# Kernel tuning notes

Hardware: AMD Instinct MI355X
Metric: run time of the kernel (lower is better)

Reference implementation:

```python
import jax, jax.numpy as jnp
import numpy as np

L, B, D = 512, 16, 256
H = 4            # MAX_DIFF == num_heads
MAX_BONDS = 6
MAX_DIFF = 4
PROB_SHIFT = 0.3


def _attn_weights(x, Wqk, Wq, bq, Wk, bk, mask):
    """Per-head softmax(QK^T/sqrt(hd)) with key padding mask.
    x: [b,l,d]; Wqk: [d,2d] (the inc/dec_qk pre-projection);
    Wq/Wk: [d,d] (MHA in_proj, stored x@W layout); mask: [b,l] bool (True=masked).
    Returns [b,h,l,l]. The V path / out_proj of the torch MHA are discarded
    by the original module, so they are omitted here.
    """
    b, l, d = x.shape
    hd = d // H
    q = x @ Wqk[:, :d]
    k = x @ Wqk[:, d:]
    Q = (q @ Wq + bq).reshape(b, l, H, hd)
    K = (k @ Wk + bk).reshape(b, l, H, hd)
    scores = jnp.einsum('blhd,bmhd->bhlm', Q, K) / np.sqrt(hd)
    scores = jnp.where(mask[:, None, None, :], -jnp.inf, scores)
    return jax.nn.softmax(scores, axis=-1)


def setup_inputs() -> dict:
    key = jax.random.key(0)
    ks = jax.random.split(key, 16)
    s = 0.05
    p = lambda k, shape: jax.random.normal(k, shape, jnp.float32) * s
    # key_padding_mask: last 64 positions padded (True == masked)
    src_mask = jnp.broadcast_to(jnp.arange(L)[None, :] >= (L - 64), (B, L))
    return {
        'molecule_embedding': jax.random.normal(ks[0], (L, B, D), jnp.float32),
        'src_bond': jax.random.randint(ks[1], (B, L, MAX_BONDS), 0, L, jnp.int32),
        'src_mask': src_mask,
        'W_inc_qk': p(ks[2], (D, 2 * D)),
        'Wq_inc': p(ks[3], (D, D)), 'bq_inc': p(ks[4], (D,)),
        'Wk_inc': p(ks[5], (D, D)), 'bk_inc': p(ks[6], (D,)),
        'W_dec_qk': p(ks[7], (D, 2 * D)),
        'Wq_dec': p(ks[8], (D, D)), 'bq_dec': p(ks[9], (D,)),
        'Wk_dec': p(ks[10], (D, D)), 'bk_dec': p(ks[11], (D,)),
        'Wc': p(ks[12], (MAX_DIFF, MAX_DIFF)), 'bc': p(ks[13], (MAX_DIFF,)),
    }


def reference(molecule_embedding, src_bond, src_mask,
              W_inc_qk, Wq_inc, bq_inc, Wk_inc, bk_inc,
              W_dec_qk, Wq_dec, bq_dec, Wk_dec, bk_dec,
              Wc, bc):
    x = jnp.transpose(molecule_embedding, (1, 0, 2))  # [b,l,d]
    b, l, _ = x.shape

    inc = _attn_weights(x, W_inc_qk, Wq_inc, bq_inc, Wk_inc, bk_inc, src_mask)
    dec = _attn_weights(x, W_dec_qk, Wq_dec, bq_dec, Wk_dec, bk_dec, src_mask)

    pad = (~src_mask).astype(jnp.float32)              # 1 - mask
    pm2 = pad[:, :, None] * pad[:, None, :]            # [b,l,l]

    # cls_layer((inc-dec).permute(0,2,3,1)) * (MAX_DIFF*pad_mask)[...,None]
    diff = (jnp.einsum('bhlm,hc->blmc', inc - dec, Wc) + bc)
    diff = diff * (MAX_DIFF * pm2)[..., None]          # [b,l,l,4]

    # src_bond has last dim == MAX_BONDS -> one-hot neighbor counts
    src_w = jax.nn.one_hot(src_bond, l, dtype=jnp.float32).sum(axis=2) * pm2  # [b,l,l]
    eye = jnp.eye(l, dtype=jnp.float32)
    src_w = src_w * (1.0 - eye)[None]                  # zero diagonal

    # _shift_probs(src_weight.long(), prob_shift, MAX_DIFF)
    oh = jax.nn.one_hot(src_w.astype(jnp.int32), MAX_DIFF, dtype=jnp.float32)
    probs = oh * (1.0 - PROB_SHIFT) + (1.0 - oh) * (PROB_SHIFT / (MAX_DIFF - 1))
    probs = probs / probs.sum(axis=-1, keepdims=True)

    return jnp.log(probs + 1e-6) + diff                # [b,l,l,4]
```

## Files before the change

### kernel.cpp

```cpp
#include <hip/hip_runtime.h>
#include <stdint.h>

typedef unsigned short u16t;
typedef short s8v __attribute__((ext_vector_type(8)));
typedef float f4v __attribute__((ext_vector_type(4)));

#define MFMA16 __builtin_amdgcn_mfma_f32_16x16x32_bf16
#define QKN (16*4*512*64)

__device__ __forceinline__ u16t f2bf(float f) {
  unsigned u = __builtin_bit_cast(unsigned, f);
  u += 0x7fffu + ((u >> 16) & 1u);
  return (u16t)(u >> 16);
}

__global__ __launch_bounds__(256) void prep_kernel(
    const float* __restrict__ Wiqk, const float* __restrict__ Wqi, const float* __restrict__ Wki,
    const float* __restrict__ Wdqk, const float* __restrict__ Wqd, const float* __restrict__ Wkd,
    u16t* __restrict__ weffT, const int* __restrict__ mraw, int* __restrict__ mdst) {
  __shared__ float At[16][65];
  __shared__ float Bt[16][65];
  __shared__ int mode;
  const int tid = threadIdx.x;

  if (blockIdx.z == 4) {
    if (tid == 0) mode = 0;
    __syncthreads();
    unsigned v0 = (unsigned)mraw[tid], v1 = (unsigned)mraw[tid + 256];
    if (v0 == 0x3F800000u || v1 == 0x3F800000u) mode = 2;
    __syncthreads();
    if (mode == 0 && (v0 > 1u || v1 > 1u)) mode = 1;
    __syncthreads();
    const int g = blockIdx.y * 4 + blockIdx.x;
#pragma unroll
    for (int i = 0; i < 2; ++i) {
      int idx = g * 512 + i * 256 + tid;
      int m;
      if (mode == 2)      m = (((const float*)mraw)[idx] != 0.0f) ? 1 : 0;
      else if (mode == 1) m = ((const unsigned char*)mraw)[idx];
      else                m = mraw[idx];
      mdst[idx] = m;
    }
    return;
  }

  const int n0 = blockIdx.x * 64;
  const int d0 = blockIdx.y * 64;
  const int p  = blockIdx.z;
  const float* A2  = (p == 0) ? Wqi : (p == 1) ? Wki : (p == 2) ? Wqd : Wkd;
  const float* Wqk = (p < 2) ? Wiqk : Wdqk;
  const int aoff = (p & 1) * 256;
  const int tx = tid & 15, ty = tid >> 4;

  float acc[4][4];
#pragma unroll
  for (int i = 0; i < 4; ++i)
#pragma unroll
    for (int j = 0; j < 4; ++j) acc[i][j] = 0.f;

  for (int k0 = 0; k0 < 256; k0 += 16) {
    __syncthreads();
    {
      int nn = tid & 63, kr = tid >> 6;
#pragma unroll
      for (int pass = 0; pass < 4; ++pass) {
        int kk = kr + pass * 4;
        At[kk][nn] = A2[(size_t)(k0 + kk) * 256 + n0 + nn];
      }
      int kk = tid & 15, dr = tid >> 4;
#pragma unroll
      for (int pass = 0; pass < 4; ++pass) {
        int dd = dr + pass * 16;
        Bt[kk][dd] = Wqk[(size_t)(d0 + dd) * 512 + aoff + k0 + kk];
      }
    }
    __syncthreads();
#pragma unroll
    for (int kk = 0; kk < 16; ++kk) {
      float a[4], b[4];
#pragma unroll
      for (int i = 0; i < 4; ++i) a[i] = At[kk][ty * 4 + i];
#pragma unroll
      for (int j = 0; j < 4; ++j) b[j] = Bt[kk][tx * 4 + j];
#pragma unroll
      for (int i = 0; i < 4; ++i)
#pragma unroll
        for (int j = 0; j < 4; ++j) acc[i][j] = fmaf(a[i], b[j], acc[i][j]);
    }
  }

#pragma unroll
  for (int i = 0; i < 4; ++i) {
    u16t h[4] = {f2bf(acc[i][0]), f2bf(acc[i][1]), f2bf(acc[i][2]), f2bf(acc[i][3])};
    *(uint2*)(&weffT[((size_t)(p * 256 + n0 + ty * 4 + i)) * 256 + d0 + tx * 4]) =
        *(const uint2*)h;
  }
}

__global__ __launch_bounds__(256) void proj_kernel(
    const float* __restrict__ emb, const u16t* __restrict__ weffT,
    const float* __restrict__ bq_inc, const float* __restrict__ bk_inc,
    const float* __restrict__ bq_dec, const float* __restrict__ bk_dec,
    u16t* __restrict__ qk) {
  __shared__ __align__(16) u16t As[128 * 40];
  __shared__ __align__(16) u16t Bs[128 * 40];
  const int t = threadIdx.x;
  const int n0 = blockIdx.x * 128;
  const int r0 = blockIdx.y * 128;
  const int bb = r0 >> 9;
  const int l0 = r0 & 511;
  const int lane = t & 63, wid = t >> 6;
  const int quad = lane >> 4, c15 = lane & 15;
  const int wm = wid >> 1, wn = wid & 1;

  f4v acc[4][4];
#pragma unroll
  for (int i = 0; i < 4; ++i)
#pragma unroll
    for (int j = 0; j < 4; ++j) acc[i][j] = f4v{0.f, 0.f, 0.f, 0.f};

  for (int k0 = 0; k0 < 256; k0 += 32) {
    __syncthreads();
#pragma unroll
    for (int i = 0; i < 2; ++i) {
      int c = t + i * 256;
      int m = c >> 2, off = (c & 3) * 8;
      const float* src = emb + (size_t)((l0 + m) * 16 + bb) * 256 + k0 + off;
      float4 x0 = *(const float4*)src;
      float4 x1 = *(const float4*)(src + 4);
      u16t h[8] = {f2bf(x0.x), f2bf(x0.y), f2bf(x0.z), f2bf(x0.w),
                   f2bf(x1.x), f2bf(x1.y), f2bf(x1.z), f2bf(x1.w)};
      *(uint4*)(&As[m * 40 + off]) = *(const uint4*)h;
      *(uint4*)(&Bs[m * 40 + off]) =
          *(const uint4*)(weffT + (size_t)(n0 + m) * 256 + k0 + off);
    }
    __syncthreads();
    s8v af[4], bf[4];
#pragma unroll
    for (int mi = 0; mi < 4; ++mi)
      af[mi] = *(const s8v*)(&As[(wm * 64 + mi * 16 + c15) * 40 + quad * 8]);
#pragma unroll
    for (int ni = 0; ni < 4; ++ni)
      bf[ni] = *(const s8v*)(&Bs[(wn * 64 + ni * 16 + c15) * 40 + quad * 8]);
#pragma unroll
    for (int mi = 0; mi < 4; ++mi)
#pragma unroll
      for (int ni = 0; ni < 4; ++ni)
        acc[mi][ni] = MFMA16(af[mi], bf[ni], acc[mi][ni], 0, 0, 0);
  }

  const float* biasP[4] = {bq_inc, bk_inc, bq_dec, bk_dec};
#pragma unroll
  for (int ni = 0; ni < 4; ++ni) {
    int n = n0 + wn * 64 + ni * 16 + c15;
    int p = n >> 8, h = (n >> 6) & 3, tt = n & 63, jj = n & 255;
    float bias = biasP[p][jj];
    u16t* dst = qk + (size_t)p * QKN;
#pragma unroll
    for (int mi = 0; mi < 4; ++mi) {
#pragma unroll
      for (int reg = 0; reg < 4; ++reg) {
        int l = l0 + wm * 64 + mi * 16 + quad * 4 + reg;
        dst[((size_t)(bb * 4 + h) * 512 + l) * 64 + tt] = f2bf(acc[mi][ni][reg] + bias);
      }
    }
  }
}

__global__ __launch_bounds__(512) void fused_kernel(
    const u16t* __restrict__ qk, const int* __restrict__ mask,
    const int* __restrict__ src_bond, const float* __restrict__ Wc,
    const float* __restrict__ bc, float* __restrict__ out) {
  __shared__ __align__(16) u16t Qs[8 * 16 * 72];
  __shared__ int bondsL[96];
  __shared__ int mlds[512 + 16];
  __shared__ __align__(16) float rpart[2][16][8];
  __shared__ float wlds[16];
  const int t = threadIdx.x;

  const int f = (int)(blockIdx.x + gridDim.x * blockIdx.y);
  const int j = f >> 3;
  const int bb = (f & 7) * 2 + (j >> 5);
  const int l0 = (j & 31) * 16;

#pragma unroll
  for (int i = 0; i < 2; ++i) {
    int c = t + i * 512;
    int q = c >> 7, row = (c >> 3) & 15, off = (c & 7) * 8;
    const u16t* Qb = qk + (size_t)(2 * (q >> 2)) * QKN;
    *(uint4*)(&Qs[(q * 16 + row) * 72 + off]) =
        *(const uint4*)(Qb + ((size_t)(bb * 4 + (q & 3)) * 512 + l0 + row) * 64 + off);
  }
  mlds[t] = mask[bb * 512 + t];
  if (t < 16) mlds[512 + t] = mask[bb * 512 + l0 + t];
  if (t < 96) bondsL[t] = src_bond[(size_t)(bb * 512 + l0 + t / 6) * 6 + (t % 6)];
  if (t >= 96 && t < 112) wlds[t - 96] = Wc[t - 96];

  const int lane = t & 63, wid = t >> 6;
  const int quad = lane >> 4, c15 = lane & 15;
  const int mbase = wid * 64 + c15;

  float dacc[4][4][4];
#pragma unroll
  for (int nt = 0; nt < 4; ++nt)
#pragma unroll
    for (int r = 0; r < 4; ++r)
#pragma unroll
      for (int c = 0; c < 4; ++c) dacc[nt][r][c] = 0.f;

  s8v kb0[4], kb1[4];
  {
    const u16t* Kb = qk + (size_t)1 * QKN + (size_t)(bb * 4 + 0) * 512 * 64;
#pragma unroll
    for (int nt = 0; nt < 4; ++nt) {
      const u16t* row = Kb + (size_t)(mbase + nt * 16) * 64 + quad * 8;
      kb0[nt] = *(const s8v*)row;
      kb1[nt] = *(const s8v*)(row + 32);
    }
  }

  __syncthreads();

  bool mskm[4];
#pragma unroll
  for (int nt = 0; nt < 4; ++nt) mskm[nt] = (mlds[mbase + nt * 16] != 0);

#pragma unroll 1
  for (int q = 0; q < 8; ++q) {
    const int pp = q >> 2, h = q & 3;
    s8v a0 = *(const s8v*)(&Qs[(q * 16 + c15) * 72 + quad * 8]);
    s8v a1 = *(const s8v*)(&Qs[(q * 16 + c15) * 72 + 32 + quad * 8]);

    float wv[4];
#pragma unroll
    for (int c = 0; c < 4; ++c) wv[c] = wlds[h * 4 + c];

    float E[4][4];
    float rsum[4] = {0.f, 0.f, 0.f, 0.f};
#pragma unroll
    for (int nt = 0; nt < 4; ++nt) {
      f4v sacc = f4v{0.f, 0.f, 0.f, 0.f};
      sacc = MFMA16(a0, kb0[nt], sacc, 0, 0, 0);
      sacc = MFMA16(a1, kb1[nt], sacc, 0, 0, 0);
#pragma unroll
      for (int reg = 0; reg < 4; ++reg) {
        float e = mskm[nt] ? 0.f : __expf(sacc[reg] * 0.125f);
        E[nt][reg] = e;
        rsum[reg] += e;
      }
    }

    if (q < 7) {
      const int qn = q + 1;
      const u16t* Kb = qk + (size_t)(2 * (qn >> 2) + 1) * QKN
                          + (size_t)(bb * 4 + (qn & 3)) * 512 * 64;
#pragma unroll
      for (int nt = 0; nt < 4; ++nt) {
        const u16t* row = Kb + (size_t)(mbase + nt * 16) * 64 + quad * 8;
        kb0[nt] = *(const s8v*)row;
        kb1[nt] = *(const s8v*)(row + 32);
      }
    }

#pragma unroll
    for (int reg = 0; reg < 4; ++reg) {
#pragma unroll
      for (int off = 1; off < 16; off <<= 1) rsum[reg] += __shfl_xor(rsum[reg], off);
    }
    if (c15 == 0) {
#pragma unroll
      for (int reg = 0; reg < 4; ++reg) rpart[q & 1][quad * 4 + reg][wid] = rsum[reg];
    }
    __syncthreads();

    float inv[4];
    const float sgn = pp ? -1.f : 1.f;
#pragma unroll
    for (int reg = 0; reg < 4; ++reg) {
      const float4* rp = (const float4*)&rpart[q & 1][quad * 4 + reg][0];
      float4 s0 = rp[0], s1 = rp[1];
      inv[reg] = sgn / (s0.x + s0.y + s0.z + s0.w + s1.x + s1.y + s1.z + s1.w);
    }

#pragma unroll
    for (int nt = 0; nt < 4; ++nt) {
#pragma unroll
      for (int reg = 0; reg < 4; ++reg) {
        float P = E[nt][reg] * inv[reg];
#pragma unroll
        for (int c = 0; c < 4; ++c)
          dacc[nt][reg][c] = fmaf(P, wv[c], dacc[nt][reg][c]);
      }
    }
  }

  float bcF[4];
#pragma unroll
  for (int c = 0; c < 4; ++c) bcF[c] = bc[c];
  const float lgH = logf(0.7f + 1e-6f);
  const float lgM = logf(0.1f + 1e-6f);
  const float lgU = logf(0.25f + 1e-6f);

#pragma unroll
  for (int nt = 0; nt < 4; ++nt) {
    int m = mbase + nt * 16;
    bool padm = !mskm[nt];
#pragma unroll
    for (int reg = 0; reg < 4; ++reg) {
      int lloc = quad * 4 + reg;
      int l = l0 + lloc;
      bool padl = (mlds[512 + lloc] == 0);
      bool pm = padl && padm;
      int cnt = 0;
#pragma unroll
      for (int j6 = 0; j6 < 6; ++j6) cnt += (bondsL[lloc * 6 + j6] == m) ? 1 : 0;
      int cls = (pm && (m != l)) ? cnt : 0;
      float v[4];
#pragma unroll
      for (int c = 0; c < 4; ++c) {
        float lp = (cls >= 4) ? lgU : ((c == cls) ? lgH : lgM);
        float dv = pm ? 4.f * (dacc[nt][reg][c] + bcF[c]) : 0.f;
        v[c] = lp + dv;
      }
      float4 o = make_float4(v[0], v[1], v[2], v[3]);
      *(float4*)(&out[((size_t)(bb * 512 + l) * 512 + m) * 4]) = o;
    }
  }
}

extern "C" void kernel_launch(void* const* d_in, const int* in_sizes, int n_in,
                              void* d_out, int out_size, void* d_ws, size_t ws_size,
                              hipStream_t stream) {
  (void)in_sizes; (void)n_in; (void)out_size; (void)ws_size;
  const float* emb      = (const float*)d_in[0];
  const int*   src_bond = (const int*)d_in[1];
  const int*   mask_raw = (const int*)d_in[2];
  const float* W_inc_qk = (const float*)d_in[3];
  const float* Wq_inc   = (const float*)d_in[4];
  const float* bq_inc   = (const float*)d_in[5];
  const float* Wk_inc   = (const float*)d_in[6];
  const float* bk_inc   = (const float*)d_in[7];
  const float* W_dec_qk = (const float*)d_in[8];
  const float* Wq_dec   = (const float*)d_in[9];
  const float* bq_dec   = (const float*)d_in[10];
  const float* Wk_dec   = (const float*)d_in[11];
  const float* bk_dec   = (const float*)d_in[12];
  const float* Wc       = (const float*)d_in[13];
  const float* bc       = (const float*)d_in[14];
  float* out = (float*)d_out;

  char* ws = (char*)d_ws;
  int*   wsMask = (int*)ws;
  u16t*  weffT  = (u16t*)(ws + 32768);
  u16t*  qk     = (u16t*)(ws + 32768 + 524288);

  hipLaunchKernelGGL(prep_kernel, dim3(4, 4, 5), dim3(256), 0, stream,
                     W_inc_qk, Wq_inc, Wk_inc, W_dec_qk, Wq_dec, Wk_dec, weffT,
                     mask_raw, wsMask);
  hipLaunchKernelGGL(proj_kernel, dim3(8, 64), dim3(256), 0, stream,
                     emb, weffT, bq_inc, bk_inc, bq_dec, bk_dec, qk);
  hipLaunchKernelGGL(fused_kernel, dim3(32, 16), dim3(512), 0, stream,
                     qk, wsMask, src_bond, Wc, bc, out);
}
```

Measured before the change: 175.1 us.

## Fold softmax scale into Q, accumulate per-head diffs, remap proj blocks by XCD

The 1/sqrt(hd) scale is now applied to Q in the projection epilogue, so the fused kernel skips a multiply per score. The fused kernel accumulates inc-dec probabilities per head and applies the 4x4 classifier once at the end, instead of doing 16 FMAs per q-iteration. Other changes: the q loop is fully unrolled, division becomes a fast reciprocal, the barrier waits only on LDS traffic, projection blocks are remapped for XCD locality, and bf16 conversion uses a packed hardware instruction. The risks are higher register pressure from the unroll and slightly different rounding from rcp and the scale folding.

```diff
diff --git a/kernel.cpp b/kernel.cpp
--- a/kernel.cpp
+++ b/kernel.cpp
@@ -105,8 +105,12 @@
   __shared__ __align__(16) u16t As[128 * 40];
   __shared__ __align__(16) u16t Bs[128 * 40];
   const int t = threadIdx.x;
-  const int n0 = blockIdx.x * 128;
-  const int r0 = blockIdx.y * 128;
+  const int f = (int)(blockIdx.x + gridDim.x * blockIdx.y);
+  const int xcd = f & 7, idx = f >> 3;
+  const int ry = xcd * 8 + (idx & 7);
+  const int nx = idx >> 3;
+  const int n0 = nx * 128;
+  const int r0 = ry * 128;
   const int bb = r0 >> 9;
   const int l0 = r0 & 511;
   const int lane = t & 63, wid = t >> 6;
@@ -128,9 +132,13 @@
       const float* src = emb + (size_t)((l0 + m) * 16 + bb) * 256 + k0 + off;
       float4 x0 = *(const float4*)src;
       float4 x1 = *(const float4*)(src + 4);
-      u16t h[8] = {f2bf(x0.x), f2bf(x0.y), f2bf(x0.z), f2bf(x0.w),
-                   f2bf(x1.x), f2bf(x1.y), f2bf(x1.z), f2bf(x1.w)};
-      *(uint4*)(&As[m * 40 + off]) = *(const uint4*)h;
+      unsigned p0, p1, p2, p3;
+      asm("v_cvt_pk_bf16_f32 %0, %1, %2" : "=v"(p0) : "v"(x0.x), "v"(x0.y));
+      asm("v_cvt_pk_bf16_f32 %0, %1, %2" : "=v"(p1) : "v"(x0.z), "v"(x0.w));
+      asm("v_cvt_pk_bf16_f32 %0, %1, %2" : "=v"(p2) : "v"(x1.x), "v"(x1.y));
+      asm("v_cvt_pk_bf16_f32 %0, %1, %2" : "=v"(p3) : "v"(x1.z), "v"(x1.w));
+      uint4 pk = make_uint4(p0, p1, p2, p3);
+      *(uint4*)(&As[m * 40 + off]) = pk;
       *(uint4*)(&Bs[m * 40 + off]) =
           *(const uint4*)(weffT + (size_t)(n0 + m) * 256 + k0 + off);
     }
@@ -155,13 +163,15 @@
     int n = n0 + wn * 64 + ni * 16 + c15;
     int p = n >> 8, h = (n >> 6) & 3, tt = n & 63, jj = n & 255;
     float bias = biasP[p][jj];
+    const float osc = (p & 1) ? 1.0f : 0.125f;
     u16t* dst = qk + (size_t)p * QKN;
 #pragma unroll
     for (int mi = 0; mi < 4; ++mi) {
 #pragma unroll
       for (int reg = 0; reg < 4; ++reg) {
         int l = l0 + wm * 64 + mi * 16 + quad * 4 + reg;
-        dst[((size_t)(bb * 4 + h) * 512 + l) * 64 + tt] = f2bf(acc[mi][ni][reg] + bias);
+        dst[((size_t)(bb * 4 + h) * 512 + l) * 64 + tt] =
+            f2bf((acc[mi][ni][reg] + bias) * osc);
       }
     }
   }
@@ -175,13 +185,18 @@
   __shared__ int bondsL[96];
   __shared__ int mlds[512 + 16];
   __shared__ __align__(16) float rpart[2][16][8];
-  __shared__ float wlds[16];
   const int t = threadIdx.x;
 
   const int f = (int)(blockIdx.x + gridDim.x * blockIdx.y);
   const int j = f >> 3;
   const int bb = (f & 7) * 2 + (j >> 5);
   const int l0 = (j & 31) * 16;
+
+  const int lane = t & 63, wid = t >> 6;
+  const int quad = lane >> 4, c15 = lane & 15;
+  const int mbase = wid * 64 + c15;
+  const u16t* Kblk = qk + (size_t)(bb * 4) * 512 * 64;
+  const int loff = mbase * 64 + quad * 8;
 
 #pragma unroll
   for (int i = 0; i < 2; ++i) {
@@ -194,28 +209,14 @@
   mlds[t] = mask[bb * 512 + t];
   if (t < 16) mlds[512 + t] = mask[bb * 512 + l0 + t];
   if (t < 96) bondsL[t] = src_bond[(size_t)(bb * 512 + l0 + t / 6) * 6 + (t % 6)];
-  if (t >= 96 && t < 112) wlds[t - 96] = Wc[t - 96];
-
-  const int lane = t & 63, wid = t >> 6;
-  const int quad = lane >> 4, c15 = lane & 15;
-  const int mbase = wid * 64 + c15;
-
-  float dacc[4][4][4];
-#pragma unroll
-  for (int nt = 0; nt < 4; ++nt)
-#pragma unroll
-    for (int r = 0; r < 4; ++r)
-#pragma unroll
-      for (int c = 0; c < 4; ++c) dacc[nt][r][c] = 0.f;
 
   s8v kb0[4], kb1[4];
   {
-    const u16t* Kb = qk + (size_t)1 * QKN + (size_t)(bb * 4 + 0) * 512 * 64;
+    const u16t* Kq = Kblk + (size_t)1 * QKN;
 #pragma unroll
     for (int nt = 0; nt < 4; ++nt) {
-      const u16t* row = Kb + (size_t)(mbase + nt * 16) * 64 + quad * 8;
-      kb0[nt] = *(const s8v*)row;
-      kb1[nt] = *(const s8v*)(row + 32);
+      kb0[nt] = *(const s8v*)(Kq + loff + nt * 1024);
+      kb1[nt] = *(const s8v*)(Kq + loff + nt * 1024 + 32);
     }
   }
 
@@ -225,43 +226,51 @@
 #pragma unroll
   for (int nt = 0; nt < 4; ++nt) mskm[nt] = (mlds[mbase + nt * 16] != 0);
 
-#pragma unroll 1
+  float hacc[4][4][4];
+#pragma unroll
+  for (int nt = 0; nt < 4; ++nt)
+#pragma unroll
+    for (int r = 0; r < 4; ++r)
+#pragma unroll
+      for (int h = 0; h < 4; ++h) hacc[nt][r][h] = 0.f;
+
+#pragma unroll
   for (int q = 0; q < 8; ++q) {
-    const int pp = q >> 2, h = q & 3;
+    const int h = q & 3;
     s8v a0 = *(const s8v*)(&Qs[(q * 16 + c15) * 72 + quad * 8]);
     s8v a1 = *(const s8v*)(&Qs[(q * 16 + c15) * 72 + 32 + quad * 8]);
 
-    float wv[4];
-#pragma unroll
-    for (int c = 0; c < 4; ++c) wv[c] = wlds[h * 4 + c];
-
-    float E[4][4];
-    float rsum[4] = {0.f, 0.f, 0.f, 0.f};
+    f4v s[4];
 #pragma unroll
     for (int nt = 0; nt < 4; ++nt) {
       f4v sacc = f4v{0.f, 0.f, 0.f, 0.f};
       sacc = MFMA16(a0, kb0[nt], sacc, 0, 0, 0);
       sacc = MFMA16(a1, kb1[nt], sacc, 0, 0, 0);
+      s[nt] = sacc;
+    }
+
+    if (q < 7) {
+      const int qn = q + 1;
+      const u16t* Kq = Kblk + (size_t)(2 * (qn >> 2) + 1) * QKN
+                            + (size_t)(qn & 3) * (512 * 64);
+#pragma unroll
+      for (int nt = 0; nt < 4; ++nt) {
+        kb0[nt] = *(const s8v*)(Kq + loff + nt * 1024);
+        kb1[nt] = *(const s8v*)(Kq + loff + nt * 1024 + 32);
+      }
+    }
+
+    float E[4][4];
+    float rsum[4] = {0.f, 0.f, 0.f, 0.f};
+#pragma unroll
+    for (int nt = 0; nt < 4; ++nt) {
 #pragma unroll
       for (int reg = 0; reg < 4; ++reg) {
-        float e = mskm[nt] ? 0.f : __expf(sacc[reg] * 0.125f);
+        float e = mskm[nt] ? 0.f : __expf(s[nt][reg]);
         E[nt][reg] = e;
         rsum[reg] += e;
       }
     }
-
-    if (q < 7) {
-      const int qn = q + 1;
-      const u16t* Kb = qk + (size_t)(2 * (qn >> 2) + 1) * QKN
-                          + (size_t)(bb * 4 + (qn & 3)) * 512 * 64;
-#pragma unroll
-      for (int nt = 0; nt < 4; ++nt) {
-        const u16t* row = Kb + (size_t)(mbase + nt * 16) * 64 + quad * 8;
-        kb0[nt] = *(const s8v*)row;
-        kb1[nt] = *(const s8v*)(row + 32);
-      }
-    }
-
 #pragma unroll
     for (int reg = 0; reg < 4; ++reg) {
 #pragma unroll
@@ -271,32 +280,34 @@
 #pragma unroll
       for (int reg = 0; reg < 4; ++reg) rpart[q & 1][quad * 4 + reg][wid] = rsum[reg];
     }
-    __syncthreads();
+
+    asm volatile("s_waitcnt lgkmcnt(0)" ::: "memory");
+    __builtin_amdgcn_s_barrier();
+    asm volatile("" ::: "memory");
 
     float inv[4];
-    const float sgn = pp ? -1.f : 1.f;
 #pragma unroll
     for (int reg = 0; reg < 4; ++reg) {
       const float4* rp = (const float4*)&rpart[q & 1][quad * 4 + reg][0];
       float4 s0 = rp[0], s1 = rp[1];
-      inv[reg] = sgn / (s0.x + s0.y + s0.z + s0.w + s1.x + s1.y + s1.z + s1.w);
-    }
-
-#pragma unroll
-    for (int nt = 0; nt < 4; ++nt) {
-#pragma unroll
-      for (int reg = 0; reg < 4; ++reg) {
-        float P = E[nt][reg] * inv[reg];
-#pragma unroll
-        for (int c = 0; c < 4; ++c)
-          dacc[nt][reg][c] = fmaf(P, wv[c], dacc[nt][reg][c]);
-      }
-    }
-  }
-
-  float bcF[4];
-#pragma unroll
-  for (int c = 0; c < 4; ++c) bcF[c] = bc[c];
+      float tot = s0.x + s0.y + s0.z + s0.w + s1.x + s1.y + s1.z + s1.w;
+      float r = __builtin_amdgcn_rcpf(tot);
+      inv[reg] = (q >= 4) ? -r : r;
+    }
+
+#pragma unroll
+    for (int nt = 0; nt < 4; ++nt)
+#pragma unroll
+      for (int reg = 0; reg < 4; ++reg)
+        hacc[nt][reg][h] = fmaf(E[nt][reg], inv[reg], hacc[nt][reg][h]);
+  }
+
+  float wv4[16];
+#pragma unroll
+  for (int i = 0; i < 16; ++i) wv4[i] = 4.f * Wc[i];
+  float bc4[4];
+#pragma unroll
+  for (int c = 0; c < 4; ++c) bc4[c] = 4.f * bc[c];
   const float lgH = logf(0.7f + 1e-6f);
   const float lgM = logf(0.1f + 1e-6f);
   const float lgU = logf(0.25f + 1e-6f);
@@ -318,9 +329,12 @@
       float v[4];
 #pragma unroll
       for (int c = 0; c < 4; ++c) {
+        float dv = bc4[c];
+#pragma unroll
+        for (int h = 0; h < 4; ++h)
+          dv = fmaf(hacc[nt][reg][h], wv4[h * 4 + c], dv);
         float lp = (cls >= 4) ? lgU : ((c == cls) ? lgH : lgM);
-        float dv = pm ? 4.f * (dacc[nt][reg][c] + bcF[c]) : 0.f;
-        v[c] = lp + dv;
+        v[c] = lp + (pm ? dv : 0.f);
       }
       float4 o = make_float4(v[0], v[1], v[2], v[3]);
       *(float4*)(&out[((size_t)(bb * 512 + l) * 512 + m) * 4]) = o;
```

New measurement: 213.4 us. +21.8%, slower.
